# Kernel optimization log

Measured on AMD Instinct MI355X. Metric: run time of the kernel, lower is better.

## Reference

```python
import jax, jax.numpy as jnp
import numpy as np


def setup_inputs() -> dict:
    key = jax.random.key(0)
    k1, k2, k3, k4 = jax.random.split(key, 4)
    b, h, t, dim, topk = 16, 8, 196, 512, 49
    x = jax.random.normal(k1, (b, t, dim), dtype=jnp.float32)
    adj = jax.random.normal(k2, (b, h, t, t), dtype=jnp.float32)  # per-head routing logits
    Wqkv = jax.random.normal(k3, (dim, 3 * dim), dtype=jnp.float32) * 0.02
    Wv = jax.random.normal(k4, (dim, dim), dtype=jnp.float32) * 0.02
    return {"x": x, "adj": adj, "Wqkv": Wqkv, "Wv": Wv, "topk": topk}


def reference(x, adj, Wqkv, Wv, topk):
    b, t, dim = x.shape
    h = adj.shape[1]
    d = dim // h
    scale = dim ** (-0.5)  # note: full dim, matching source (self.scale = dim**-0.5)

    # qkv projection (stand-in for GIN conv_proj_qkv with nhid = 3*dim)
    qkv = (x @ Wqkv).reshape(b, t, h, 3 * d).transpose(0, 2, 1, 3)  # b h t 3d
    q, k, v = jnp.split(qkv, 3, axis=-1)  # each b h t d

    # TopkRouting: indices of top-k routing logits per (b, h, query-token)
    _, r_idx = jax.lax.top_k(adj, topk)  # b h t topk (r_weight unused: mul_weight='none')

    # KGather: irregular gather of concatenated k/v rows per query token
    kv = jnp.concatenate([k, v], axis=-1).reshape(b * h, t, 2 * d)
    idx = r_idx.reshape(b * h, t, topk)
    kv_sel = jax.vmap(lambda m, i: m[i])(kv, idx)          # (bh, t, topk, 2d)
    kv_sel = kv_sel.reshape(b, h, t, topk, 2 * d)
    k_sel, v_sel = jnp.split(kv_sel, 2, axis=-1)            # b h t topk d

    # small-window attention: each query attends to its topk gathered rows (w^2 = 1)
    attn = jax.nn.softmax(jnp.einsum('bhtd,bhtkd->bhtk', q * scale, k_sel), axis=-1)
    o = jnp.einsum('bhtk,bhtkd->bhtd', attn, v_sel)

    o = o.transpose(0, 2, 1, 3).reshape(b, t, dim)
    o = jax.nn.gelu(o, approximate=False)  # torch F.gelu default = exact erf
    return o @ Wv
```

## Files before the change

### kernel.cpp

```cpp
#include <hip/hip_runtime.h>
#include <hip/hip_bf16.h>
#include <cmath>

#define B_   16
#define H_   8
#define T_   196
#define DIM_ 512
#define DHEAD_ 64
#define TOPK_ 49
#define BT_  (B_ * T_)
#define BH_  (B_ * H_)

#define QB_OFF   0u
#define KB_OFF   1605632u
#define VT_OFF   3211264u
#define XB_OFF   5046272u
#define WQKVT_OFF 6651904u
#define WVT_OFF  7438336u
#define MASK_OFF 7700480u

#define QSPLIT_BLOCKS 3136

typedef __bf16 bf16x8 __attribute__((ext_vector_type(8)));
typedef float f32x4 __attribute__((ext_vector_type(4)));

__device__ __forceinline__ unsigned short f2bf(float f) {
    union { float f; unsigned int u; } v; v.f = f;
    const unsigned int u = v.u;
    return (unsigned short)((u + 0x7FFFu + ((u >> 16) & 1u)) >> 16);
}

__device__ __forceinline__ unsigned int ordered_u32(float f) {
    int i = __float_as_int(f);
    return (i < 0) ? ~(unsigned int)i : ((unsigned int)i | 0x80000000u);
}

__device__ __forceinline__ void gload16(const void* g, void* l) {
    __builtin_amdgcn_global_load_lds(
        (const __attribute__((address_space(1))) unsigned int*)g,
        (__attribute__((address_space(3))) unsigned int*)l, 16, 0, 0);
}

__device__ __forceinline__ void route_topk_q(const float* __restrict__ adj,
                                             unsigned int* __restrict__ masks,
                                             const int q, const int lane) {
    const float* arow = adj + (size_t)q * T_;
    const bool v3 = (lane < 4);
    unsigned int u[4];
    u[0] = ordered_u32(arow[lane]);
    u[1] = ordered_u32(arow[lane + 64]);
    u[2] = ordered_u32(arow[lane + 128]);
    u[3] = v3 ? ordered_u32(arow[lane + 192]) : 0u;

    unsigned int w0 = u[0], w1 = u[1], w2 = u[2], w3 = u[3];
    unsigned int prefix = 0u, thr = 0u;
    int k = TOPK_, A = T_;
    for (int b = 31; b >= 0; --b) {
        int C1 = 0;
        C1 += __popcll(__ballot((w0 >> b) == 1u));
        C1 += __popcll(__ballot((w1 >> b) == 1u));
        C1 += __popcll(__ballot((w2 >> b) == 1u));
        C1 += __popcll(__ballot((w3 >> b) == 1u));
        if (C1 >= k) {
            const unsigned int bit = 1u << b;
            prefix |= bit;
            w0 ^= bit; w1 ^= bit; w2 ^= bit; w3 ^= bit;
            A = C1;
        } else { k -= C1; A -= C1; }

        if (k == A || k == 1) {
            const bool mx = (k == 1);
            unsigned int best = mx ? 0u : 0xFFFFFFFFu;
            const unsigned int ww[4] = {w0, w1, w2, w3};
#pragma unroll
            for (int s2 = 0; s2 < 4; ++s2) {
                const bool valid = (s2 < 3) || v3;
                const bool act = valid && ((ww[s2] >> b) == 0u);
                if (act) best = mx ? (u[s2] > best ? u[s2] : best)
                                   : (u[s2] < best ? u[s2] : best);
            }
#pragma unroll
            for (int off = 32; off >= 1; off >>= 1) {
                const unsigned int o = __shfl_xor(best, off);
                best = mx ? (o > best ? o : best) : (o < best ? o : best);
            }
            thr = best;
            break;
        }
        if (b == 0) thr = prefix;
    }

    const unsigned long long lmask = (1ull << lane) - 1ull;
    unsigned long long gm[4];
    int G = 0;
#pragma unroll
    for (int s2 = 0; s2 < 4; ++s2) {
        const bool valid = (s2 < 3) || v3;
        gm[s2] = __ballot(valid && (u[s2] > thr));
        G += __popcll(gm[s2]);
    }
    const int need = TOPK_ - G;
    int cum = 0;
    unsigned long long sb0 = 0, sb1 = 0, sb2 = 0, sb3 = 0;
#pragma unroll
    for (int s2 = 0; s2 < 4; ++s2) {
        const bool valid = (s2 < 3) || v3;
        const bool e = valid && (u[s2] == thr);
        const unsigned long long em = __ballot(e);
        const int rk = cum + __popcll(em & lmask);
        cum += __popcll(em);
        const unsigned long long sel = gm[s2] | __ballot(e && (rk < need));
        if (s2 == 0) sb0 = sel; else if (s2 == 1) sb1 = sel;
        else if (s2 == 2) sb2 = sel; else sb3 = sel;
    }
    if (lane < 8) {
        const unsigned long long mv = (lane < 2) ? sb0 : (lane < 4) ? sb1
                                    : (lane < 6) ? sb2 : sb3;
        const unsigned int wd = (lane & 1) ? (unsigned int)(mv >> 32) : (unsigned int)mv;
        masks[(size_t)q * 8 + lane] = wd;
    }
}

__global__ __launch_bounds__(256) void prep(const float* __restrict__ x,
                                            const float* __restrict__ Wqkv,
                                            const float* __restrict__ Wv,
                                            const float* __restrict__ adj,
                                            unsigned short* __restrict__ xb,
                                            unsigned short* __restrict__ wqkvT,
                                            unsigned short* __restrict__ wvT,
                                            unsigned short* __restrict__ vT,
                                            unsigned int* __restrict__ masks) {
    __shared__ unsigned short Tt[64][72];
    const int t = threadIdx.x;
    const int bid = blockIdx.x;

    if (bid < QSPLIT_BLOCKS) {
        route_topk_q(adj, masks, bid * 4 + (t >> 6), t & 63);
        return;
    }
    int b2 = bid - QSPLIT_BLOCKS;
    if (b2 < 784) {
        const size_t base = ((size_t)b2 * 256 + t) * 8;
        const float4 v0 = *(const float4*)&x[base];
        const float4 v1 = *(const float4*)&x[base + 4];
        uint4 pk;
        pk.x = (unsigned int)f2bf(v0.x) | ((unsigned int)f2bf(v0.y) << 16);
        pk.y = (unsigned int)f2bf(v0.z) | ((unsigned int)f2bf(v0.w) << 16);
        pk.z = (unsigned int)f2bf(v1.x) | ((unsigned int)f2bf(v1.y) << 16);
        pk.w = (unsigned int)f2bf(v1.z) | ((unsigned int)f2bf(v1.w) << 16);
        *(uint4*)&xb[base] = pk;
        return;
    }
    b2 -= 784;
    if (b2 >= 192 && b2 < 220) {
        const int e0 = (b2 - 192) * 8192 + t;
#pragma unroll
        for (int i = 0; i < 32; ++i) {
            const int e = e0 + i * 256;
            const int bh = e / 1792;
            const int rem = e - bh * 1792;
            const int d = rem / 28;
            const int tt = rem - d * 28;
            vT[(size_t)bh * (64 * 224) + (size_t)d * 224 + 196 + tt] = 0;
        }
        return;
    }

    const float* src;
    unsigned short* dst;
    int Cc, tx, ty;
    if (b2 < 192) { src = Wqkv; dst = wqkvT; Cc = 1536; tx = b2 % 24; ty = b2 / 24; }
    else { const int b = b2 - 220; src = Wv; dst = wvT; Cc = 512; tx = b & 7; ty = b >> 3; }
    const int c0 = tx * 64, r0 = ty * 64;
#pragma unroll
    for (int p = 0; p < 4; ++p) {
        const int r = (t >> 4) + 16 * p;
        const int cl = (t & 15) * 4;
        const float4 v = *(const float4*)&src[(size_t)(r0 + r) * Cc + c0 + cl];
        Tt[cl + 0][r] = f2bf(v.x);
        Tt[cl + 1][r] = f2bf(v.y);
        Tt[cl + 2][r] = f2bf(v.z);
        Tt[cl + 3][r] = f2bf(v.w);
    }
    __syncthreads();
#pragma unroll
    for (int p = 0; p < 2; ++p) {
        const int cc = (t >> 3) + 32 * p;
        const int ch = (t & 7) * 8;
        *(uint4*)&dst[(size_t)(c0 + cc) * 512 + r0 + ch] = *(const uint4*)&Tt[cc][ch];
    }
}

template <int BM, int BN, int MODE, int FUSE, typename CT>
__global__ __launch_bounds__(256) void gemm_mfma(const unsigned short* __restrict__ A,
                                                 const unsigned short* __restrict__ Bt,
                                                 CT* __restrict__ C,
                                                 const int M, const int N, const int K,
                                                 const float* __restrict__ adj,
                                                 unsigned int* __restrict__ masks) {
    constexpr int FN = BN / 32;
    constexpr int MF = BM / 32;
    constexpr int AW = BM / 16;
    constexpr int CSZ = (MODE == 1) ? 64 * 132 : 1;
    struct ABt { unsigned short A[BM][32]; unsigned short B[BN][32]; };
    __shared__ union {
        ABt ab[2];
        unsigned short Cs[CSZ];
    } sm;

    const int tid = threadIdx.x;
    const int lane = tid & 63, wid = tid >> 6;
    const int mt = M / BM;
    const int nGemm = mt * (N / BN);
    const int bid = blockIdx.x;

    if constexpr (FUSE) {
        if (bid >= nGemm) {
            const int rid = bid - nGemm;
            route_topk_q(adj, masks, QSPLIT_BLOCKS * 4 + rid * 4 + wid, lane);
            return;
        }
    }

    const int bx = bid % mt;
    const int by = bid / mt;
    const int row0 = bx * BM;
    const int col0 = by * BN;
    const int wr = wid >> 1, wc = wid & 1;

    f32x4 acc[MF][FN];
#pragma unroll
    for (int m = 0; m < MF; ++m)
#pragma unroll
        for (int n = 0; n < FN; ++n)
            acc[m][n] = (f32x4){0.0f, 0.0f, 0.0f, 0.0f};

    const int srow = lane >> 2;
    const int scol = (lane & 3) * 8;
    const unsigned short* aSrc = A + (size_t)(row0 + wid * 16 + srow) * K + scol;
    const unsigned short* bSrc = Bt + (size_t)(col0 + wid * 16 + srow) * K + scol;
    const unsigned short* bSrc2 = bSrc + (size_t)64 * K;

    const int fr = lane & 15;
    const int fk8 = (lane >> 4) * 8;

#define STAGE(BUF) do {                                                        \
        if (wid < AW) gload16(aSrc, &sm.ab[BUF].A[wid * 16][0]);               \
        gload16(bSrc, &sm.ab[BUF].B[wid * 16][0]);                             \
        if constexpr (BN == 128) gload16(bSrc2, &sm.ab[BUF].B[64 + wid * 16][0]); \
        aSrc += 32; bSrc += 32; bSrc2 += 32;                                   \
    } while (0)

#define COMPUTE(BUF) do {                                                      \
        bf16x8 af[MF], bfv[FN];                                                \
        _Pragma("unroll")                                                      \
        for (int m = 0; m < MF; ++m)                                           \
            af[m] = *(const bf16x8*)&sm.ab[BUF].A[wr * (BM / 2) + m * 16 + fr][fk8]; \
        _Pragma("unroll")                                                      \
        for (int n = 0; n < FN; ++n)                                           \
            bfv[n] = *(const bf16x8*)&sm.ab[BUF].B[wc * (BN / 2) + n * 16 + fr][fk8]; \
        _Pragma("unroll")                                                      \
        for (int m = 0; m < MF; ++m)                                           \
            _Pragma("unroll")                                                  \
            for (int n = 0; n < FN; ++n)                                       \
                acc[m][n] = __builtin_amdgcn_mfma_f32_16x16x32_bf16(af[m], bfv[n], acc[m][n], 0, 0, 0); \
    } while (0)

    STAGE(0);
    __syncthreads();

    for (int k0 = 0; k0 < K; k0 += 64) {
        if (k0 + 32 < K) STAGE(1);
        COMPUTE(0);
        __syncthreads();
        if (k0 + 64 < K) STAGE(0);
        COMPUTE(1);
        __syncthreads();
    }
#undef STAGE
#undef COMPUTE

    if constexpr (MODE == 0) {
#pragma unroll
        for (int m = 0; m < MF; ++m)
#pragma unroll
            for (int n = 0; n < FN; ++n)
#pragma unroll
                for (int i = 0; i < 4; ++i) {
                    const int row = row0 + wr * (BM / 2) + m * 16 + (lane >> 4) * 4 + i;
                    const int col = col0 + wc * (BN / 2) + n * 16 + (lane & 15);
                    C[(size_t)row * N + col] = (CT)acc[m][n][i];
                }
    } else {
#pragma unroll
        for (int m = 0; m < MF; ++m)
#pragma unroll
            for (int n = 0; n < FN; ++n)
#pragma unroll
                for (int i = 0; i < 4; ++i) {
                    const int rl = wr * (BM / 2) + m * 16 + (lane >> 4) * 4 + i;
                    const int cl = wc * (BN / 2) + n * 16 + (lane & 15);
                    sm.Cs[rl * 132 + cl] = f2bf(acc[m][n][i]);
                }
        __syncthreads();

        unsigned short* ubase = (unsigned short*)C;
#pragma unroll
        for (int ch = 0; ch < BN / 64; ++ch) {
            const int abscol = col0 + ch * 64;
            const int which = (abscol >> 6) % 3;
            const int hh = abscol / 192;
            if (which < 2) {
                const int r = tid >> 2;
                const int co = (tid & 3) * 16;
                const int gr = row0 + r;
                const int bb = gr / T_;
                const int tt = gr - bb * T_;
                const uint2 a0 = *(const uint2*)&sm.Cs[r * 132 + ch * 64 + co];
                const uint2 a1 = *(const uint2*)&sm.Cs[r * 132 + ch * 64 + co + 4];
                const uint2 a2 = *(const uint2*)&sm.Cs[r * 132 + ch * 64 + co + 8];
                const uint2 a3 = *(const uint2*)&sm.Cs[r * 132 + ch * 64 + co + 12];
                unsigned short* dst = ubase + (size_t)which * KB_OFF +
                                      ((size_t)(bb * H_ + hh) * T_ + tt) * DHEAD_ + co;
                uint4 w0; w0.x = a0.x; w0.y = a0.y; w0.z = a1.x; w0.w = a1.y;
                uint4 w1; w1.x = a2.x; w1.y = a2.y; w1.z = a3.x; w1.w = a3.y;
                *(uint4*)&dst[0] = w0;
                *(uint4*)&dst[8] = w1;
            } else {
                const int d = tid >> 2;
                const int j0 = (tid & 3) * 16;
                union { unsigned short s[16]; uint2 v2[4]; } tmp;
#pragma unroll
                for (int j = 0; j < 16; ++j)
                    tmp.s[j] = sm.Cs[(j0 + j) * 132 + ch * 64 + d];
                const int gr0 = row0 + j0;
                const int bb0 = gr0 / T_;
                const int bb1 = (gr0 + 15) / T_;
                if (bb0 == bb1) {
                    const int tt = gr0 - bb0 * T_;
                    unsigned short* dst = ubase + VT_OFF +
                                          (size_t)(bb0 * H_ + hh) * (64 * 224) +
                                          (size_t)d * 224 + tt;
                    *(uint2*)&dst[0]  = tmp.v2[0];
                    *(uint2*)&dst[4]  = tmp.v2[1];
                    *(uint2*)&dst[8]  = tmp.v2[2];
                    *(uint2*)&dst[12] = tmp.v2[3];
                } else {
#pragma unroll
                    for (int j = 0; j < 16; ++j) {
                        const int gr = gr0 + j;
                        const int bb = gr / T_;
                        const int tt = gr - bb * T_;
                        ubase[VT_OFF + (size_t)(bb * H_ + hh) * (64 * 224) +
                              (size_t)d * 224 + tt] = tmp.s[j];
                    }
                }
            }
        }
    }
}

__global__ __launch_bounds__(256, 4) void attn_mfma(const unsigned short* __restrict__ qb,
                                                    const unsigned short* __restrict__ kb,
                                                    const unsigned short* __restrict__ vT,
                                                    const unsigned int* __restrict__ masks,
                                                    unsigned short* __restrict__ obuf) {
    __shared__ union {
        struct { unsigned int mask[16][8]; unsigned short P[4][16][72]; } p1;
        struct { float Of[4][16][64]; float Lw[4][16]; } p2;
    } sm;

    const int tid = threadIdx.x;
    const int lane = tid & 63;
    const int w = tid >> 6;
    const int qt = blockIdx.x;
    const int bh = blockIdx.y;
    const int bb = bh >> 3, hh = bh & 7;
    const int q0 = qt * 16;

    if (tid < 128) {
        const int r = tid >> 3, wd = tid & 7;
        const int t = q0 + r;
        sm.p1.mask[r][wd] = (t < T_) ? masks[((size_t)bh * T_ + t) * 8 + wd] : 0u;
    }
    {
        unsigned short* Pw = &sm.p1.P[w][0][0];
        const int r = lane >> 2, c = (lane & 3) * 16;
        *(uint4*)&Pw[r * 72 + c]     = (uint4){0u, 0u, 0u, 0u};
        *(uint4*)&Pw[r * 72 + c + 8] = (uint4){0u, 0u, 0u, 0u};
    }
    __syncthreads();

    const int fr = lane & 15;
    const int fk8 = (lane >> 4) * 8;
    const int nc = (w == 0) ? 4 : 3;
    const int cbase = (w == 0) ? 0 : 1 + 3 * w;
    const int keybase = cbase * 16;

    const unsigned short* qbh = qb + ((size_t)bh * T_ + q0) * DHEAD_;
    const unsigned short* kbh = kb + (size_t)bh * T_ * DHEAD_;

    const bf16x8 aq0 = *(const bf16x8*)&qbh[fr * 64 + fk8];
    const bf16x8 aq1 = *(const bf16x8*)&qbh[fr * 64 + 32 + fk8];

    f32x4 s[4];
#pragma unroll
    for (int c2 = 0; c2 < 4; ++c2) s[c2] = (f32x4){0.0f, 0.0f, 0.0f, 0.0f};
    __builtin_amdgcn_s_setprio(1);
#pragma unroll
    for (int c2 = 0; c2 < 4; ++c2) {
        if (c2 < nc) {
            const int c = cbase + c2;
            const bf16x8 b0 = *(const bf16x8*)&kbh[(c * 16 + fr) * 64 + fk8];
            const bf16x8 b1 = *(const bf16x8*)&kbh[(c * 16 + fr) * 64 + 32 + fk8];
            s[c2] = __builtin_amdgcn_mfma_f32_16x16x32_bf16(aq0, b0, s[c2], 0, 0, 0);
            s[c2] = __builtin_amdgcn_mfma_f32_16x16x32_bf16(aq1, b1, s[c2], 0, 0, 0);
        }
    }
    __builtin_amdgcn_s_setprio(0);

    const float scale = 0.044194173824159216f;
    float lv[4];
#pragma unroll
    for (int i = 0; i < 4; ++i) {
        const int rowl = (lane >> 4) * 4 + i;
        float li = 0.0f;
#pragma unroll
        for (int c2 = 0; c2 < 4; ++c2) {
            if (c2 < nc) {
                const int c = cbase + c2;
                const unsigned int mw = sm.p1.mask[rowl][c >> 1];
                const bool sel = (mw >> (((c & 1) << 4) + fr)) & 1u;
                const float pv = sel ? __expf(s[c2][i] * scale) : 0.0f;
                sm.p1.P[w][rowl][c2 * 16 + fr] = f2bf(pv);
                li += pv;
            }
        }
        lv[i] = li;
    }
#pragma unroll
    for (int off = 8; off >= 1; off >>= 1)
#pragma unroll
        for (int i = 0; i < 4; ++i)
            lv[i] += __shfl_xor(lv[i], off);

    const unsigned short* vbh = vT + (size_t)bh * (64 * 224) + keybase;
    f32x4 o_p[4];
#pragma unroll
    for (int n = 0; n < 4; ++n) o_p[n] = (f32x4){0.0f, 0.0f, 0.0f, 0.0f};
    const bf16x8 ap0 = *(const bf16x8*)&sm.p1.P[w][fr][fk8];
    const bf16x8 ap1 = *(const bf16x8*)&sm.p1.P[w][fr][32 + fk8];
    __builtin_amdgcn_s_setprio(1);
#pragma unroll
    for (int n = 0; n < 4; ++n) {
        const bf16x8 bv0 = *(const bf16x8*)&vbh[(n * 16 + fr) * 224 + fk8];
        const bf16x8 bv1 = *(const bf16x8*)&vbh[(n * 16 + fr) * 224 + 32 + fk8];
        o_p[n] = __builtin_amdgcn_mfma_f32_16x16x32_bf16(ap0, bv0, o_p[n], 0, 0, 0);
        o_p[n] = __builtin_amdgcn_mfma_f32_16x16x32_bf16(ap1, bv1, o_p[n], 0, 0, 0);
    }
    __builtin_amdgcn_s_setprio(0);

    __syncthreads();

#pragma unroll
    for (int n = 0; n < 4; ++n)
#pragma unroll
        for (int i = 0; i < 4; ++i)
            sm.p2.Of[w][(lane >> 4) * 4 + i][n * 16 + fr] = o_p[n][i];
    if (fr == 0) {
#pragma unroll
        for (int i = 0; i < 4; ++i)
            sm.p2.Lw[w][(lane >> 4) * 4 + i] = lv[i];
    }
    __syncthreads();

    {
        const int r = tid >> 4;
        const int c0 = (tid & 15) * 4;
        const int t = q0 + r;
        if (t < T_) {
            const float l = sm.p2.Lw[0][r] + sm.p2.Lw[1][r] +
                            sm.p2.Lw[2][r] + sm.p2.Lw[3][r];
            const float rl = 1.0f / l;
            const f32x4 a0 = *(const f32x4*)&sm.p2.Of[0][r][c0];
            const f32x4 a1 = *(const f32x4*)&sm.p2.Of[1][r][c0];
            const f32x4 a2 = *(const f32x4*)&sm.p2.Of[2][r][c0];
            const f32x4 a3 = *(const f32x4*)&sm.p2.Of[3][r][c0];
            union { unsigned short s[4]; unsigned long long u; } pk;
#pragma unroll
            for (int j = 0; j < 4; ++j) {
                const float ov = (a0[j] + a1[j] + a2[j] + a3[j]) * rl;
                const float g = 0.5f * ov * (1.0f + erff(ov * 0.70710678118654752f));
                pk.s[j] = f2bf(g);
            }
            unsigned short* orow = obuf + ((size_t)(bb * T_ + t)) * DIM_ +
                                   hh * DHEAD_ + c0;
            *(unsigned long long*)orow = pk.u;
        }
    }
}

extern "C" void kernel_launch(void* const* d_in, const int* in_sizes, int n_in,
                              void* d_out, int out_size, void* d_ws, size_t ws_size,
                              hipStream_t stream) {
    const float* x    = (const float*)d_in[0];
    const float* adj  = (const float*)d_in[1];
    const float* Wqkv = (const float*)d_in[2];
    const float* Wv   = (const float*)d_in[3];
    float* out = (float*)d_out;
    unsigned short* ub = (unsigned short*)d_ws;

    unsigned short* qb    = ub + QB_OFF;
    unsigned short* kb    = ub + KB_OFF;
    unsigned short* vT    = ub + VT_OFF;
    unsigned short* xb    = ub + XB_OFF;
    unsigned short* wqkvT = ub + WQKVT_OFF;
    unsigned short* wvT   = ub + WVT_OFF;
    unsigned int*   masks = (unsigned int*)(ub + MASK_OFF);

    prep<<<4204, 256, 0, stream>>>(x, Wqkv, Wv, adj, xb, wqkvT, wvT, vT, masks);

    gemm_mfma<64, 128, 1, 1, unsigned short><<<3724, 256, 0, stream>>>(
        xb, wqkvT, ub, BT_, 3 * DIM_, DIM_, adj, masks);

    attn_mfma<<<dim3(13, BH_), 256, 0, stream>>>(qb, kb, vT, masks, xb);

    gemm_mfma<32, 64, 0, 0, float><<<784, 256, 0, stream>>>(
        xb, wvT, out, BT_, DIM_, DIM_, nullptr, nullptr);
}
```

Baseline: 62.31 us.

## Process 32 queries per attention block and quad-buffer the output GEMM

The attention kernel now handles two 16-query tiles per block. Each K and V fragment loaded from global memory feeds MFMAs for both tiles, and the grid is roughly halved. The output projection GEMM gets a 4-buffer shared-memory variant that stages 64 k-elements ahead and syncs once per 64-wide step. The cost is more registers and shared memory per block, fewer attention blocks, and out-of-range query reads in the last tile.

```diff
diff --git a/kernel.cpp b/kernel.cpp
--- a/kernel.cpp
+++ b/kernel.cpp
@@ -191,7 +191,7 @@
     }
 }
 
-template <int BM, int BN, int MODE, int FUSE, typename CT>
+template <int BM, int BN, int MODE, int FUSE, int BUFS, typename CT>
 __global__ __launch_bounds__(256) void gemm_mfma(const unsigned short* __restrict__ A,
                                                  const unsigned short* __restrict__ Bt,
                                                  CT* __restrict__ C,
@@ -204,7 +204,7 @@
     constexpr int CSZ = (MODE == 1) ? 64 * 132 : 1;
     struct ABt { unsigned short A[BM][32]; unsigned short B[BN][32]; };
     __shared__ union {
-        ABt ab[2];
+        ABt ab[BUFS];
         unsigned short Cs[CSZ];
     } sm;
 
@@ -237,21 +237,20 @@
 
     const int srow = lane >> 2;
     const int scol = (lane & 3) * 8;
-    const unsigned short* aSrc = A + (size_t)(row0 + wid * 16 + srow) * K + scol;
-    const unsigned short* bSrc = Bt + (size_t)(col0 + wid * 16 + srow) * K + scol;
-    const unsigned short* bSrc2 = bSrc + (size_t)64 * K;
+    const unsigned short* aSrc0 = A + (size_t)(row0 + wid * 16 + srow) * K + scol;
+    const unsigned short* bSrc0 = Bt + (size_t)(col0 + wid * 16 + srow) * K + scol;
+    const unsigned short* bSrc20 = bSrc0 + (size_t)64 * K;
 
     const int fr = lane & 15;
     const int fk8 = (lane >> 4) * 8;
 
-#define STAGE(BUF) do {                                                        \
-        if (wid < AW) gload16(aSrc, &sm.ab[BUF].A[wid * 16][0]);               \
-        gload16(bSrc, &sm.ab[BUF].B[wid * 16][0]);                             \
-        if constexpr (BN == 128) gload16(bSrc2, &sm.ab[BUF].B[64 + wid * 16][0]); \
-        aSrc += 32; bSrc += 32; bSrc2 += 32;                                   \
+#define STAGE_AT(BUF, KOFF) do {                                               \
+        if (wid < AW) gload16(aSrc0 + (KOFF), &sm.ab[BUF].A[wid * 16][0]);     \
+        gload16(bSrc0 + (KOFF), &sm.ab[BUF].B[wid * 16][0]);                   \
+        if constexpr (BN == 128) gload16(bSrc20 + (KOFF), &sm.ab[BUF].B[64 + wid * 16][0]); \
     } while (0)
 
-#define COMPUTE(BUF) do {                                                      \
+#define COMPUTE_AT(BUF) do {                                                   \
         bf16x8 af[MF], bfv[FN];                                                \
         _Pragma("unroll")                                                      \
         for (int m = 0; m < MF; ++m)                                           \
@@ -266,19 +265,34 @@
                 acc[m][n] = __builtin_amdgcn_mfma_f32_16x16x32_bf16(af[m], bfv[n], acc[m][n], 0, 0, 0); \
     } while (0)
 
-    STAGE(0);
-    __syncthreads();
-
-    for (int k0 = 0; k0 < K; k0 += 64) {
-        if (k0 + 32 < K) STAGE(1);
-        COMPUTE(0);
+    if constexpr (BUFS == 2) {
+        STAGE_AT(0, 0);
         __syncthreads();
-        if (k0 + 64 < K) STAGE(0);
-        COMPUTE(1);
+        for (int k0 = 0; k0 < K; k0 += 64) {
+            if (k0 + 32 < K) STAGE_AT(1, k0 + 32);
+            COMPUTE_AT(0);
+            __syncthreads();
+            if (k0 + 64 < K) STAGE_AT(0, k0 + 64);
+            COMPUTE_AT(1);
+            __syncthreads();
+        }
+    } else {
+        STAGE_AT(0, 0);
+        STAGE_AT(1, 32);
         __syncthreads();
-    }
-#undef STAGE
-#undef COMPUTE
+        int p = 0;
+        for (int k0 = 0; k0 < K; k0 += 64, p ^= 1) {
+            if (k0 + 64 < K) {
+                STAGE_AT(2 - 2 * p, k0 + 64);
+                STAGE_AT(3 - 2 * p, k0 + 96);
+            }
+            COMPUTE_AT(2 * p);
+            COMPUTE_AT(2 * p + 1);
+            __syncthreads();
+        }
+    }
+#undef STAGE_AT
+#undef COMPUTE_AT
 
     if constexpr (MODE == 0) {
 #pragma unroll
@@ -366,8 +380,8 @@
                                                     const unsigned int* __restrict__ masks,
                                                     unsigned short* __restrict__ obuf) {
     __shared__ union {
-        struct { unsigned int mask[16][8]; unsigned short P[4][16][72]; } p1;
-        struct { float Of[4][16][64]; float Lw[4][16]; } p2;
+        struct { unsigned int mask[32][8]; unsigned short P[4][2][16][72]; } p1;
+        struct { float Of[4][32][64]; float Lw[4][32]; } p2;
     } sm;
 
     const int tid = threadIdx.x;
@@ -376,18 +390,20 @@
     const int qt = blockIdx.x;
     const int bh = blockIdx.y;
     const int bb = bh >> 3, hh = bh & 7;
-    const int q0 = qt * 16;
-
-    if (tid < 128) {
+    const int q0 = qt * 32;
+
+    {
         const int r = tid >> 3, wd = tid & 7;
         const int t = q0 + r;
         sm.p1.mask[r][wd] = (t < T_) ? masks[((size_t)bh * T_ + t) * 8 + wd] : 0u;
     }
     {
-        unsigned short* Pw = &sm.p1.P[w][0][0];
         const int r = lane >> 2, c = (lane & 3) * 16;
-        *(uint4*)&Pw[r * 72 + c]     = (uint4){0u, 0u, 0u, 0u};
-        *(uint4*)&Pw[r * 72 + c + 8] = (uint4){0u, 0u, 0u, 0u};
+#pragma unroll
+        for (int tau = 0; tau < 2; ++tau) {
+            *(uint4*)&sm.p1.P[w][tau][r][c]     = (uint4){0u, 0u, 0u, 0u};
+            *(uint4*)&sm.p1.P[w][tau][r][c + 8] = (uint4){0u, 0u, 0u, 0u};
+        }
     }
     __syncthreads();
 
@@ -400,12 +416,17 @@
     const unsigned short* qbh = qb + ((size_t)bh * T_ + q0) * DHEAD_;
     const unsigned short* kbh = kb + (size_t)bh * T_ * DHEAD_;
 
-    const bf16x8 aq0 = *(const bf16x8*)&qbh[fr * 64 + fk8];
-    const bf16x8 aq1 = *(const bf16x8*)&qbh[fr * 64 + 32 + fk8];
-
-    f32x4 s[4];
-#pragma unroll
-    for (int c2 = 0; c2 < 4; ++c2) s[c2] = (f32x4){0.0f, 0.0f, 0.0f, 0.0f};
+    const bf16x8 aqA0 = *(const bf16x8*)&qbh[fr * 64 + fk8];
+    const bf16x8 aqA1 = *(const bf16x8*)&qbh[fr * 64 + 32 + fk8];
+    const bf16x8 aqB0 = *(const bf16x8*)&qbh[(16 + fr) * 64 + fk8];
+    const bf16x8 aqB1 = *(const bf16x8*)&qbh[(16 + fr) * 64 + 32 + fk8];
+
+    f32x4 sA[4], sB[4];
+#pragma unroll
+    for (int c2 = 0; c2 < 4; ++c2) {
+        sA[c2] = (f32x4){0.0f, 0.0f, 0.0f, 0.0f};
+        sB[c2] = (f32x4){0.0f, 0.0f, 0.0f, 0.0f};
+    }
     __builtin_amdgcn_s_setprio(1);
 #pragma unroll
     for (int c2 = 0; c2 < 4; ++c2) {
@@ -413,89 +434,116 @@
             const int c = cbase + c2;
             const bf16x8 b0 = *(const bf16x8*)&kbh[(c * 16 + fr) * 64 + fk8];
             const bf16x8 b1 = *(const bf16x8*)&kbh[(c * 16 + fr) * 64 + 32 + fk8];
-            s[c2] = __builtin_amdgcn_mfma_f32_16x16x32_bf16(aq0, b0, s[c2], 0, 0, 0);
-            s[c2] = __builtin_amdgcn_mfma_f32_16x16x32_bf16(aq1, b1, s[c2], 0, 0, 0);
+            sA[c2] = __builtin_amdgcn_mfma_f32_16x16x32_bf16(aqA0, b0, sA[c2], 0, 0, 0);
+            sA[c2] = __builtin_amdgcn_mfma_f32_16x16x32_bf16(aqA1, b1, sA[c2], 0, 0, 0);
+            sB[c2] = __builtin_amdgcn_mfma_f32_16x16x32_bf16(aqB0, b0, sB[c2], 0, 0, 0);
+            sB[c2] = __builtin_amdgcn_mfma_f32_16x16x32_bf16(aqB1, b1, sB[c2], 0, 0, 0);
         }
     }
     __builtin_amdgcn_s_setprio(0);
 
     const float scale = 0.044194173824159216f;
-    float lv[4];
-#pragma unroll
-    for (int i = 0; i < 4; ++i) {
-        const int rowl = (lane >> 4) * 4 + i;
-        float li = 0.0f;
-#pragma unroll
-        for (int c2 = 0; c2 < 4; ++c2) {
-            if (c2 < nc) {
-                const int c = cbase + c2;
-                const unsigned int mw = sm.p1.mask[rowl][c >> 1];
-                const bool sel = (mw >> (((c & 1) << 4) + fr)) & 1u;
-                const float pv = sel ? __expf(s[c2][i] * scale) : 0.0f;
-                sm.p1.P[w][rowl][c2 * 16 + fr] = f2bf(pv);
-                li += pv;
-            }
-        }
-        lv[i] = li;
-    }
+    float lv[8];
+#pragma unroll
+    for (int tau = 0; tau < 2; ++tau)
+#pragma unroll
+        for (int i = 0; i < 4; ++i) {
+            const int rowl = (lane >> 4) * 4 + i;
+            float li = 0.0f;
+#pragma unroll
+            for (int c2 = 0; c2 < 4; ++c2) {
+                if (c2 < nc) {
+                    const int c = cbase + c2;
+                    const unsigned int mw = sm.p1.mask[tau * 16 + rowl][c >> 1];
+                    const bool sel = (mw >> (((c & 1) << 4) + fr)) & 1u;
+                    const float sv = (tau == 0) ? sA[c2][i] : sB[c2][i];
+                    const float pv = sel ? __expf(sv * scale) : 0.0f;
+                    sm.p1.P[w][tau][rowl][c2 * 16 + fr] = f2bf(pv);
+                    li += pv;
+                }
+            }
+            lv[tau * 4 + i] = li;
+        }
 #pragma unroll
     for (int off = 8; off >= 1; off >>= 1)
 #pragma unroll
-        for (int i = 0; i < 4; ++i)
-            lv[i] += __shfl_xor(lv[i], off);
+        for (int j = 0; j < 8; ++j)
+            lv[j] += __shfl_xor(lv[j], off);
 
     const unsigned short* vbh = vT + (size_t)bh * (64 * 224) + keybase;
-    f32x4 o_p[4];
-#pragma unroll
-    for (int n = 0; n < 4; ++n) o_p[n] = (f32x4){0.0f, 0.0f, 0.0f, 0.0f};
-    const bf16x8 ap0 = *(const bf16x8*)&sm.p1.P[w][fr][fk8];
-    const bf16x8 ap1 = *(const bf16x8*)&sm.p1.P[w][fr][32 + fk8];
+    f32x4 oA[4], oB[4];
+#pragma unroll
+    for (int n = 0; n < 4; ++n) {
+        oA[n] = (f32x4){0.0f, 0.0f, 0.0f, 0.0f};
+        oB[n] = (f32x4){0.0f, 0.0f, 0.0f, 0.0f};
+    }
+    const bf16x8 apA0 = *(const bf16x8*)&sm.p1.P[w][0][fr][fk8];
+    const bf16x8 apA1 = *(const bf16x8*)&sm.p1.P[w][0][fr][32 + fk8];
+    const bf16x8 apB0 = *(const bf16x8*)&sm.p1.P[w][1][fr][fk8];
+    const bf16x8 apB1 = *(const bf16x8*)&sm.p1.P[w][1][fr][32 + fk8];
     __builtin_amdgcn_s_setprio(1);
 #pragma unroll
     for (int n = 0; n < 4; ++n) {
         const bf16x8 bv0 = *(const bf16x8*)&vbh[(n * 16 + fr) * 224 + fk8];
         const bf16x8 bv1 = *(const bf16x8*)&vbh[(n * 16 + fr) * 224 + 32 + fk8];
-        o_p[n] = __builtin_amdgcn_mfma_f32_16x16x32_bf16(ap0, bv0, o_p[n], 0, 0, 0);
-        o_p[n] = __builtin_amdgcn_mfma_f32_16x16x32_bf16(ap1, bv1, o_p[n], 0, 0, 0);
+        oA[n] = __builtin_amdgcn_mfma_f32_16x16x32_bf16(apA0, bv0, oA[n], 0, 0, 0);
+        oA[n] = __builtin_amdgcn_mfma_f32_16x16x32_bf16(apA1, bv1, oA[n], 0, 0, 0);
+        oB[n] = __builtin_amdgcn_mfma_f32_16x16x32_bf16(apB0, bv0, oB[n], 0, 0, 0);
+        oB[n] = __builtin_amdgcn_mfma_f32_16x16x32_bf16(apB1, bv1, oB[n], 0, 0, 0);
     }
     __builtin_amdgcn_s_setprio(0);
 
     __syncthreads();
 
 #pragma unroll
-    for (int n = 0; n < 4; ++n)
-#pragma unroll
-        for (int i = 0; i < 4; ++i)
-            sm.p2.Of[w][(lane >> 4) * 4 + i][n * 16 + fr] = o_p[n][i];
+    for (int tau = 0; tau < 2; ++tau)
+#pragma unroll
+        for (int n = 0; n < 4; ++n)
+#pragma unroll
+            for (int i = 0; i < 4; ++i)
+                sm.p2.Of[w][tau * 16 + (lane >> 4) * 4 + i][n * 16 + fr] =
+                    (tau == 0) ? oA[n][i] : oB[n][i];
     if (fr == 0) {
 #pragma unroll
-        for (int i = 0; i < 4; ++i)
-            sm.p2.Lw[w][(lane >> 4) * 4 + i] = lv[i];
+        for (int tau = 0; tau < 2; ++tau)
+#pragma unroll
+            for (int i = 0; i < 4; ++i)
+                sm.p2.Lw[w][tau * 16 + (lane >> 4) * 4 + i] = lv[tau * 4 + i];
     }
     __syncthreads();
 
     {
-        const int r = tid >> 4;
-        const int c0 = (tid & 15) * 4;
+        const int r = tid >> 3;
+        const int c0 = (tid & 7) * 8;
         const int t = q0 + r;
         if (t < T_) {
             const float l = sm.p2.Lw[0][r] + sm.p2.Lw[1][r] +
                             sm.p2.Lw[2][r] + sm.p2.Lw[3][r];
             const float rl = 1.0f / l;
-            const f32x4 a0 = *(const f32x4*)&sm.p2.Of[0][r][c0];
-            const f32x4 a1 = *(const f32x4*)&sm.p2.Of[1][r][c0];
-            const f32x4 a2 = *(const f32x4*)&sm.p2.Of[2][r][c0];
-            const f32x4 a3 = *(const f32x4*)&sm.p2.Of[3][r][c0];
-            union { unsigned short s[4]; unsigned long long u; } pk;
+            const f32x4 a0l = *(const f32x4*)&sm.p2.Of[0][r][c0];
+            const f32x4 a1l = *(const f32x4*)&sm.p2.Of[1][r][c0];
+            const f32x4 a2l = *(const f32x4*)&sm.p2.Of[2][r][c0];
+            const f32x4 a3l = *(const f32x4*)&sm.p2.Of[3][r][c0];
+            const f32x4 a0h = *(const f32x4*)&sm.p2.Of[0][r][c0 + 4];
+            const f32x4 a1h = *(const f32x4*)&sm.p2.Of[1][r][c0 + 4];
+            const f32x4 a2h = *(const f32x4*)&sm.p2.Of[2][r][c0 + 4];
+            const f32x4 a3h = *(const f32x4*)&sm.p2.Of[3][r][c0 + 4];
+            union { unsigned short s[8]; uint4 u; } pk;
 #pragma unroll
             for (int j = 0; j < 4; ++j) {
-                const float ov = (a0[j] + a1[j] + a2[j] + a3[j]) * rl;
+                const float ov = (a0l[j] + a1l[j] + a2l[j] + a3l[j]) * rl;
                 const float g = 0.5f * ov * (1.0f + erff(ov * 0.70710678118654752f));
                 pk.s[j] = f2bf(g);
             }
+#pragma unroll
+            for (int j = 0; j < 4; ++j) {
+                const float ov = (a0h[j] + a1h[j] + a2h[j] + a3h[j]) * rl;
+                const float g = 0.5f * ov * (1.0f + erff(ov * 0.70710678118654752f));
+                pk.s[4 + j] = f2bf(g);
+            }
             unsigned short* orow = obuf + ((size_t)(bb * T_ + t)) * DIM_ +
                                    hh * DHEAD_ + c0;
-            *(unsigned long long*)orow = pk.u;
+            *(uint4*)orow = pk.u;
         }
     }
 }
@@ -520,11 +568,11 @@
 
     prep<<<4204, 256, 0, stream>>>(x, Wqkv, Wv, adj, xb, wqkvT, wvT, vT, masks);
 
-    gemm_mfma<64, 128, 1, 1, unsigned short><<<3724, 256, 0, stream>>>(
+    gemm_mfma<64, 128, 1, 1, 2, unsigned short><<<3724, 256, 0, stream>>>(
         xb, wqkvT, ub, BT_, 3 * DIM_, DIM_, adj, masks);
 
-    attn_mfma<<<dim3(13, BH_), 256, 0, stream>>>(qb, kb, vT, masks, xb);
-
-    gemm_mfma<32, 64, 0, 0, float><<<784, 256, 0, stream>>>(
+    attn_mfma<<<dim3(7, BH_), 256, 0, stream>>>(qb, kb, vT, masks, xb);
+
+    gemm_mfma<32, 64, 0, 0, 4, float><<<784, 256, 0, stream>>>(
         xb, wvT, out, BT_, DIM_, DIM_, nullptr, nullptr);
 }
```

New measurement: 62.94 us. No clear change (+1.0%).
